# Optimization experiments

Hardware: AMD Instinct MI355X
Metric: run time of the kernel (lower is better)

The kernel has to match this reference:

```python
import jax, jax.numpy as jnp
import numpy as np
import math

B, T, C = 2, 2048, 1024
NH = 16
HD = C // NH

def setup_inputs() -> dict:
    key = jax.random.key(0)
    ks = jax.random.split(key, 3)
    scale = 0.02
    return {
        "x": jax.random.normal(ks[0], (B, T, C), dtype=jnp.float32),
        "Wqkv": jax.random.normal(ks[1], (C, 3 * C), dtype=jnp.float32) * scale,
        "bqkv": jnp.zeros((3 * C,), dtype=jnp.float32),
        "Wproj": jax.random.normal(ks[2], (C, C), dtype=jnp.float32) * scale,
        "bproj": jnp.zeros((C,), dtype=jnp.float32),
    }

def reference(x, Wqkv, bqkv, Wproj, bproj):
    b, t, c = x.shape
    qkv = x @ Wqkv + bqkv                      # (B,T,3C)
    qkv = qkv.reshape(b, t, 3, NH, HD)
    q = jnp.transpose(qkv[:, :, 0], (0, 2, 1, 3))  # (B,H,T,D)
    k = jnp.transpose(qkv[:, :, 1], (0, 2, 1, 3))
    v = jnp.transpose(qkv[:, :, 2], (0, 2, 1, 3))
    att = jnp.einsum('bhqd,bhkd->bhqk', q, k) / math.sqrt(HD)
    causal = jnp.tril(jnp.ones((t, t), dtype=bool))
    att = jnp.where(causal[None, None], att, jnp.float32(-jnp.inf))
    att = jax.nn.softmax(att, axis=-1)
    y = jnp.einsum('bhqk,bhkd->bhqd', att, v)  # (B,H,T,D)
    y = jnp.transpose(y, (0, 2, 1, 3)).reshape(b, t, c)
    return y @ Wproj + bproj
```

## Files before the change

kernel.cpp:

```cpp
#include <hip/hip_runtime.h>


typedef __attribute__((ext_vector_type(8))) short short8;
typedef __attribute__((ext_vector_type(4))) short short4v;
typedef __attribute__((ext_vector_type(4))) float f32x4;
typedef __attribute__((ext_vector_type(2))) unsigned int u32x2;

#define MFMA16(a, b, c) __builtin_amdgcn_mfma_f32_16x16x32_bf16((a), (b), (c), 0, 0, 0)
#define MFMA16K16(a, b, c) __builtin_amdgcn_mfma_f32_16x16x16bf16_1k((a), (b), (c), 0, 0, 0)

__device__ __forceinline__ unsigned short f2bf(float f) {
  unsigned u = __builtin_bit_cast(unsigned, f);
  u += 0x7fffu + ((u >> 16) & 1u);
  return (unsigned short)(u >> 16);
}

__device__ __forceinline__ unsigned short f2bf_fast(float f) {
  return (unsigned short)((__builtin_bit_cast(unsigned, f) + 0x8000u) >> 16);
}

#if __has_builtin(__builtin_amdgcn_cvt_pk_bf16_f32)
typedef __attribute__((ext_vector_type(2))) __bf16 bf16x2;
__device__ __forceinline__ short4v pack_bf16x4(float a, float b, float c, float d) {
  bf16x2 lo = __builtin_amdgcn_cvt_pk_bf16_f32(a, b);
  bf16x2 hi = __builtin_amdgcn_cvt_pk_bf16_f32(c, d);
  u32x2 t;
  t[0] = __builtin_bit_cast(unsigned, lo);
  t[1] = __builtin_bit_cast(unsigned, hi);
  return __builtin_bit_cast(short4v, t);
}
#else
__device__ __forceinline__ short4v pack_bf16x4(float a, float b, float c, float d) {
  short4v r;
  r[0] = (short)f2bf_fast(a); r[1] = (short)f2bf_fast(b);
  r[2] = (short)f2bf_fast(c); r[3] = (short)f2bf_fast(d);
  return r;
}
#endif

__device__ __forceinline__ short4v pack_rne4(float a, float b, float c, float d) {
  short4v r;
  r[0] = (short)f2bf(a); r[1] = (short)f2bf(b);
  r[2] = (short)f2bf(c); r[3] = (short)f2bf(d);
  return r;
}

__device__ __forceinline__ void gl2lds16(const void* g, void* l) {
  __builtin_amdgcn_global_load_lds(
      (__attribute__((address_space(1))) void*)g,
      (__attribute__((address_space(3))) void*)l,
      16, 0, 0);
}

__global__ __launch_bounds__(256)
void prep(const float* __restrict__ x, unsigned short* __restrict__ xb,
          const float* __restrict__ Wqkv, unsigned short* __restrict__ wqkvT,
          const float* __restrict__ Wproj, unsigned short* __restrict__ wprojT) {
  __shared__ float tile[64][65];
  const int bx = blockIdx.x, tid = threadIdx.x;
  if (bx < 4096) {
    const int i = (bx * 256 + tid) * 4;
    float4 f = *(const float4*)(x + i);
    unsigned long long r = (unsigned long long)f2bf(f.x)
        | ((unsigned long long)f2bf(f.y) << 16)
        | ((unsigned long long)f2bf(f.z) << 32)
        | ((unsigned long long)f2bf(f.w) << 48);
    *(unsigned long long*)(xb + i) = r;
    return;
  }
  const float* W;
  unsigned short* WT;
  int n0, k0, N;
  if (bx < 4864) {
    const int idx = bx - 4096;
    W = Wqkv; WT = wqkvT; N = 3072;
    n0 = (idx % 48) * 64; k0 = (idx / 48) * 64;
  } else {
    const int idx = bx - 4864;
    W = Wproj; WT = wprojT; N = 1024;
    n0 = (idx % 16) * 64; k0 = (idx / 16) * 64;
  }
  const int K = 1024;
  const int c = tid & 63, rbase = tid >> 6;
#pragma unroll
  for (int i = 0; i < 16; ++i) {
    int r = i * 4 + rbase;
    tile[r][c] = W[(size_t)(k0 + r) * N + n0 + c];
  }
  __syncthreads();
#pragma unroll
  for (int i = 0; i < 16; ++i) {
    int r = i * 4 + rbase;
    WT[(size_t)(n0 + r) * K + k0 + c] = f2bf(tile[c][r]);
  }
}

template <int MT>
__device__ __forceinline__ void gemm_core(
    const unsigned short* __restrict__ gA,
    const unsigned short* __restrict__ gB,
    unsigned short* As, unsigned short* Bs,
    int Kdim, int wave, int quad, int lr, int wm, int wn,
    f32x4 (&acc)[MT / 32][4]) {
  constexpr int IF = MT / 32;
  constexpr int RA = MT / 32;
  const size_t rstep = (size_t)32 * Kdim;
  for (int k0 = 0; k0 < Kdim; k0 += 64) {
#pragma unroll
    for (int rd = 0; rd < RA; ++rd)
      gl2lds16(gA + k0 + rd * rstep, As + rd * 2048 + wave * 512);
#pragma unroll
    for (int rd = 0; rd < 4; ++rd)
      gl2lds16(gB + k0 + rd * rstep, Bs + rd * 2048 + wave * 512);
    __syncthreads();
#pragma unroll
    for (int s = 0; s < 2; ++s) {
      const int sw = ((s * 4 + quad) ^ (lr & 7)) * 8;
      short8 a[IF], b[4];
#pragma unroll
      for (int i = 0; i < IF; ++i)
        a[i] = *(const short8*)(As + (wm * (MT / 2) + i * 16 + lr) * 64 + sw);
#pragma unroll
      for (int j = 0; j < 4; ++j)
        b[j] = *(const short8*)(Bs + (wn * 64 + j * 16 + lr) * 64 + sw);
#pragma unroll
      for (int i = 0; i < IF; ++i)
#pragma unroll
        for (int j = 0; j < 4; ++j)
          acc[i][j] = MFMA16(a[i], b[j], acc[i][j]);
    }
    __syncthreads();
  }
}

template <int EPI, int MT>
__global__ __launch_bounds__(256)
void gemm_bt(const unsigned short* __restrict__ A,
             const unsigned short* __restrict__ BT,
             const float* __restrict__ bias,
             float* __restrict__ outF,
             unsigned short* __restrict__ q_out,
             unsigned short* __restrict__ k_out,
             unsigned short* __restrict__ vT_out,
             int Ndim, int Kdim) {
  constexpr int IF = MT / 32;
  __shared__ __align__(16) unsigned short As[MT * 64];
  __shared__ __align__(16) unsigned short Bs[128 * 64];
  const int tid = threadIdx.x;
  const int wave = tid >> 6, lane = tid & 63;
  const int quad = lane >> 4, lr = lane & 15;
  const int wm = wave >> 1, wn = wave & 1;
  const int m0 = blockIdx.y * MT, n0 = blockIdx.x * 128;

  const int r_l = tid >> 3;
  const int cg = (tid & 7) ^ (r_l & 7);
  const unsigned short* gA = A + (size_t)(m0 + r_l) * Kdim + cg * 8;
  const unsigned short* gB = BT + (size_t)(n0 + r_l) * Kdim + cg * 8;

  f32x4 acc[IF][4] = {};
  gemm_core<MT>(gA, gB, As, Bs, Kdim, wave, quad, lr, wm, wn, acc);

  const int row_t = wm * (MT / 2) + quad * 4;
  const int col_t = wn * 64 + lr;
  if constexpr (EPI == 0) {
    const int sec = n0 >> 10;
    const float scl = (sec == 0) ? 0.18033688f : 1.0f;
#pragma unroll
    for (int j = 0; j < 4; ++j) {
      const int n = n0 + col_t + j * 16;
      const float bi = bias[n];
      const int nn = n & 1023, h = nn >> 6, d = nn & 63;
#pragma unroll
      for (int i = 0; i < IF; ++i) {
        const int m_base = m0 + row_t + i * 16;
        const int bb = m_base >> 11, t0 = m_base & 2047;
        const int bh = bb * 16 + h;
        if (sec == 2) {
          short4v pk = pack_rne4(acc[i][j][0] + bi, acc[i][j][1] + bi,
                                 acc[i][j][2] + bi, acc[i][j][3] + bi);
          *(short4v*)(vT_out + ((size_t)bh * 64 + d) * 2048 + t0) = pk;
        } else {
          unsigned short* dst = (sec == 0 ? q_out : k_out) + (size_t)bh * 131072 + t0 * 64 + d;
#pragma unroll
          for (int r = 0; r < 4; ++r)
            dst[r * 64] = f2bf((acc[i][j][r] + bi) * scl);
        }
      }
    }
  } else {
#pragma unroll
    for (int i = 0; i < IF; ++i)
#pragma unroll
      for (int r = 0; r < 4; ++r) {
        const int m = m0 + row_t + i * 16 + r;
#pragma unroll
        for (int j = 0; j < 4; ++j) {
          const int n = n0 + col_t + j * 16;
          outF[(size_t)m * Ndim + n] = acc[i][j][r] + bias[n];
        }
      }
  }
}

__global__ __launch_bounds__(256, 4)
void attn(const unsigned short* __restrict__ qbuf,
          const unsigned short* __restrict__ kbuf,
          const unsigned short* __restrict__ vT,
          unsigned short* __restrict__ yb,
          float* __restrict__ o_part,
          float* __restrict__ l_part) {
  __shared__ __align__(16) unsigned short Ks[2][4096];
  __shared__ __align__(16) unsigned short Vs[2][4096];
  const int tid = threadIdx.x, wave = tid >> 6, lane = tid & 63;
  const int quad = lane >> 4, lr = lane & 15;
  const int bh = blockIdx.x;
  const int jj = 47 - (int)blockIdx.y;
  int qt, kstart, kend, chunk;
  if (jj >= 32)      { qt = jj - 16; chunk = 1; kstart = (qt + 1) >> 1; kend = qt + 1; }
  else if (jj >= 16) { qt = jj;      chunk = 0; kstart = 0; kend = (qt + 1) >> 1; }
  else               { qt = jj;      chunk = -1; kstart = 0; kend = qt + 1; }
  const int qrow0 = qt * 64;

  const unsigned short* qp0 = qbuf + (size_t)bh * 131072;
  const unsigned short* kp0 = kbuf + (size_t)bh * 131072;
  const unsigned short* vp0 = vT   + (size_t)bh * 131072;

  short8 aq[2];
  {
    const unsigned short* qp =
        qp0 + (size_t)(qrow0 + wave * 16 + lr) * 64 + quad * 8;
    aq[0] = *(const short8*)qp;
    aq[1] = *(const short8*)(qp + 32);
  }

  short4v ones4;
#pragma unroll
  for (int i = 0; i < 4; ++i) ones4[i] = (short)0x3F80;

  const int sr = tid >> 3;
  const int scg = (tid & 7) ^ (sr & 7);
  int kbase[2];
#pragma unroll
  for (int h = 0; h < 2; ++h)
    kbase[h] = lr * 64 + (((quad + 4 * h) ^ (lr & 7)) << 3);
  int vbase[4];
#pragma unroll
  for (int kb = 0; kb < 4; ++kb)
    vbase[kb] = lr * 64 + (((2 * kb + (quad >> 1)) ^ (lr & 7)) << 3) + (quad & 1) * 4;

  f32x4 o[4] = {};
  f32x4 lacc = {};

  auto stage = [&](int buf, int kt) {
    const unsigned short* kg = kp0 + (size_t)(kt * 64 + sr) * 64 + scg * 8;
    const unsigned short* vg = vp0 + (size_t)sr * 2048 + kt * 64 + scg * 8;
    gl2lds16(kg,             &Ks[buf][wave * 512]);
    gl2lds16(kg + 32 * 64,   &Ks[buf][2048 + wave * 512]);
    gl2lds16(vg,             &Vs[buf][wave * 512]);
    gl2lds16(vg + 32 * 2048, &Vs[buf][2048 + wave * 512]);
  };

  stage(0, kstart);
  int cur = 0;
  for (int kt = kstart; kt < kend; ++kt) {
    __builtin_amdgcn_s_waitcnt(0x0F70);
    __builtin_amdgcn_s_barrier();
    if (kt + 1 < kend) stage(cur ^ 1, kt + 1);
    const unsigned short* Kb = Ks[cur];
    const unsigned short* Vb = Vs[cur];
    short8 bk[4][2];
#pragma unroll
    for (int jt = 0; jt < 4; ++jt) {
      bk[jt][0] = *(const short8*)(Kb + jt * 1024 + kbase[0]);
      bk[jt][1] = *(const short8*)(Kb + jt * 1024 + kbase[1]);
    }
    f32x4 s[4] = {};
    __builtin_amdgcn_s_setprio(1);
#pragma unroll
    for (int jt = 0; jt < 4; ++jt) {
      s[jt] = MFMA16(bk[jt][0], aq[0], s[jt]);
      s[jt] = MFMA16(bk[jt][1], aq[1], s[jt]);
    }
    __builtin_amdgcn_s_setprio(0);
    short4v pa[4];
    if (kt == qt) {
      const int qloc = wave * 16 + lr;
#pragma unroll
      for (int jt = 0; jt < 4; ++jt) {
        float p[4];
#pragma unroll
        for (int r = 0; r < 4; ++r) {
          p[r] = __builtin_amdgcn_exp2f(s[jt][r]);
          if (jt * 16 + quad * 4 + r > qloc) p[r] = 0.f;
        }
        pa[jt] = pack_bf16x4(p[0], p[1], p[2], p[3]);
      }
    } else {
#pragma unroll
      for (int jt = 0; jt < 4; ++jt) {
        float p[4];
#pragma unroll
        for (int r = 0; r < 4; ++r) p[r] = __builtin_amdgcn_exp2f(s[jt][r]);
        pa[jt] = pack_bf16x4(p[0], p[1], p[2], p[3]);
      }
    }
    __builtin_amdgcn_s_setprio(1);
#pragma unroll
    for (int kb = 0; kb < 4; ++kb)
      lacc = MFMA16K16(ones4, pa[kb], lacc);
#pragma unroll
    for (int kb = 0; kb < 4; ++kb)
#pragma unroll
      for (int jd = 0; jd < 4; ++jd) {
        const short4v bv = *(const short4v*)(Vb + jd * 1024 + vbase[kb]);
        o[jd] = MFMA16K16(pa[kb], bv, o[jd]);
      }
    __builtin_amdgcn_s_setprio(0);
    cur ^= 1;
  }

  if (chunk < 0) {
    const int b = bh >> 4, h = bh & 15;
    float inv[4];
#pragma unroll
    for (int r = 0; r < 4; ++r)
      inv[r] = __builtin_amdgcn_rcpf(__shfl(lacc[0], quad * 4 + r));
#pragma unroll
    for (int jd = 0; jd < 4; ++jd)
#pragma unroll
      for (int r = 0; r < 4; ++r) {
        const int t = qrow0 + wave * 16 + quad * 4 + r;
        yb[((size_t)b * 2048 + t) * 1024 + h * 64 + jd * 16 + lr] =
            f2bf(o[jd][r] * inv[r]);
      }
  } else {
    const int slot = (bh * 16 + (qt - 16)) * 2 + chunk;
    float* op = o_part + ((size_t)slot * 64 + wave * 16) * 64;
#pragma unroll
    for (int jd = 0; jd < 4; ++jd)
#pragma unroll
      for (int r = 0; r < 4; ++r)
        op[(quad * 4 + r) * 64 + jd * 16 + lr] = o[jd][r];
    if (lane < 16) l_part[slot * 64 + wave * 16 + lane] = lacc[0];
  }
}

__global__ __launch_bounds__(256)
void combine(const float* __restrict__ o_part, const float* __restrict__ l_part,
             unsigned short* __restrict__ yb) {
  const int bh = blockIdx.x, qtl = blockIdx.y;
  const int tid = threadIdx.x;
  const int row = tid >> 2, dd = (tid & 3) * 16;
  const int qt = 16 + qtl;
  const int slotA = (bh * 16 + qtl) * 2, slotB = slotA + 1;
  const float l = l_part[slotA * 64 + row] + l_part[slotB * 64 + row];
  const float inv = __builtin_amdgcn_rcpf(l);
  const float* oa = o_part + ((size_t)slotA * 64 + row) * 64 + dd;
  const float* ob = o_part + ((size_t)slotB * 64 + row) * 64 + dd;
  const int b = bh >> 4, h = bh & 15;
  unsigned short* yp = yb + ((size_t)b * 2048 + qt * 64 + row) * 1024 + h * 64 + dd;
#pragma unroll
  for (int j = 0; j < 16; j += 4) {
    const float4 a4 = *(const float4*)(oa + j);
    const float4 b4 = *(const float4*)(ob + j);
    short4v pk = pack_rne4((a4.x + b4.x) * inv, (a4.y + b4.y) * inv,
                           (a4.z + b4.z) * inv, (a4.w + b4.w) * inv);
    *(short4v*)(yp + j) = pk;
  }
}

extern "C" void kernel_launch(void* const* d_in, const int* in_sizes, int n_in,
                              void* d_out, int out_size, void* d_ws, size_t ws_size,
                              hipStream_t stream) {
  const float* x     = (const float*)d_in[0];
  const float* Wqkv  = (const float*)d_in[1];
  const float* bqkv  = (const float*)d_in[2];
  const float* Wproj = (const float*)d_in[3];
  const float* bproj = (const float*)d_in[4];
  float* out = (float*)d_out;

  char* ws = (char*)d_ws;
  unsigned short* xb     = (unsigned short*)(ws);
  unsigned short* wqkvT  = (unsigned short*)(ws + 8388608);
  unsigned short* wprojT = (unsigned short*)(ws + 14680064);
  unsigned short* qbuf   = (unsigned short*)(ws + 16777216);
  unsigned short* kbuf   = (unsigned short*)(ws + 25165824);
  unsigned short* vTbuf  = (unsigned short*)(ws + 33554432);
  unsigned short* ybuf   = (unsigned short*)(ws + 41943040);
  float* o_part          = (float*)(ws + 50331648);
  float* l_part          = (float*)(ws + 67108864);

  prep<<<5120, 256, 0, stream>>>(x, xb, Wqkv, wqkvT, Wproj, wprojT);
  gemm_bt<0, 128><<<dim3(24, 32), 256, 0, stream>>>(xb, wqkvT, bqkv, nullptr,
                                                    qbuf, kbuf, vTbuf, 3072, 1024);
  attn<<<dim3(32, 48), 256, 0, stream>>>(qbuf, kbuf, vTbuf, ybuf, o_part, l_part);
  combine<<<dim3(32, 16), 256, 0, stream>>>(o_part, l_part, ybuf);
  gemm_bt<1, 64><<<dim3(8, 64), 256, 0, stream>>>(ybuf, wprojT, bproj, out,
                                                  nullptr, nullptr, nullptr, 1024, 1024);
}
```

Baseline: 176.9 us.

## Process 128 query rows per attention block and rebalance causal split-K chunks

Each attention block now handles two 64-row query groups that share every K/V tile staged in LDS, halving K/V traffic per query row. Work is split into 1 to 4 key-range chunks according to query-tile depth so blocks carry roughly equal causal work. Combine is generalized to sum a variable number of partials. In exchange the kernel needs more registers, even as the launch bounds now ask for 5 waves of occupancy, which may cause spills. It also adds a larger partial buffer and more combine traffic.

```diff
diff --git a/kernel.cpp b/kernel.cpp
--- a/kernel.cpp
+++ b/kernel.cpp
@@ -202,7 +202,7 @@
   }
 }
 
-__global__ __launch_bounds__(256, 4)
+__global__ __launch_bounds__(256, 5)
 void attn(const unsigned short* __restrict__ qbuf,
           const unsigned short* __restrict__ kbuf,
           const unsigned short* __restrict__ vT,
@@ -214,23 +214,28 @@
   const int tid = threadIdx.x, wave = tid >> 6, lane = tid & 63;
   const int quad = lane >> 4, lr = lane & 15;
   const int bh = blockIdx.x;
-  const int jj = 47 - (int)blockIdx.y;
-  int qt, kstart, kend, chunk;
-  if (jj >= 32)      { qt = jj - 16; chunk = 1; kstart = (qt + 1) >> 1; kend = qt + 1; }
-  else if (jj >= 16) { qt = jj;      chunk = 0; kstart = 0; kend = (qt + 1) >> 1; }
-  else               { qt = jj;      chunk = -1; kstart = 0; kend = qt + 1; }
-  const int qrow0 = qt * 64;
+  const int by = blockIdx.y;
+  int qt, ci, nch;
+  if (by < 16)      { qt = 12 + (by & 3); ci = by >> 2; nch = 4; }
+  else if (by < 28) { int u = by - 16; qt = 8 + (u & 3); ci = u >> 2; nch = 3; }
+  else if (by < 36) { int u = by - 28; qt = 4 + (u & 3); ci = u >> 2; nch = 2; }
+  else              { qt = by - 36; ci = 0; nch = 1; }
+  const int nt = 2 * qt + 2;
+  const int kstart = (ci * nt) / nch;
+  const int kend = ((ci + 1) * nt) / nch;
+  const int qrow0 = qt * 128;
 
   const unsigned short* qp0 = qbuf + (size_t)bh * 131072;
   const unsigned short* kp0 = kbuf + (size_t)bh * 131072;
   const unsigned short* vp0 = vT   + (size_t)bh * 131072;
 
-  short8 aq[2];
-  {
+  short8 aq[2][2];
+#pragma unroll
+  for (int g = 0; g < 2; ++g) {
     const unsigned short* qp =
-        qp0 + (size_t)(qrow0 + wave * 16 + lr) * 64 + quad * 8;
-    aq[0] = *(const short8*)qp;
-    aq[1] = *(const short8*)(qp + 32);
+        qp0 + (size_t)(qrow0 + g * 64 + wave * 16 + lr) * 64 + quad * 8;
+    aq[g][0] = *(const short8*)qp;
+    aq[g][1] = *(const short8*)(qp + 32);
   }
 
   short4v ones4;
@@ -248,8 +253,8 @@
   for (int kb = 0; kb < 4; ++kb)
     vbase[kb] = lr * 64 + (((2 * kb + (quad >> 1)) ^ (lr & 7)) << 3) + (quad & 1) * 4;
 
-  f32x4 o[4] = {};
-  f32x4 lacc = {};
+  f32x4 o[2][4] = {};
+  f32x4 lacc[2] = {};
 
   auto stage = [&](int buf, int kt) {
     const unsigned short* kg = kp0 + (size_t)(kt * 64 + sr) * 64 + scg * 8;
@@ -260,6 +265,7 @@
     gl2lds16(vg + 32 * 2048, &Vs[buf][2048 + wave * 512]);
   };
 
+  const int d0 = 2 * qt;
   stage(0, kstart);
   int cur = 0;
   for (int kt = kstart; kt < kend; ++kt) {
@@ -274,97 +280,127 @@
       bk[jt][0] = *(const short8*)(Kb + jt * 1024 + kbase[0]);
       bk[jt][1] = *(const short8*)(Kb + jt * 1024 + kbase[1]);
     }
-    f32x4 s[4] = {};
+    short4v pa[2][4];
+#pragma unroll
+    for (int g = 0; g < 2; ++g) {
+      const int dg = 2 * qt + g;
+      if (kt > dg) {
+#pragma unroll
+        for (int jt = 0; jt < 4; ++jt) pa[g][jt] = (short4v)0;
+      } else {
+        f32x4 s[4] = {};
+        __builtin_amdgcn_s_setprio(1);
+#pragma unroll
+        for (int jt = 0; jt < 4; ++jt) {
+          s[jt] = MFMA16(bk[jt][0], aq[g][0], s[jt]);
+          s[jt] = MFMA16(bk[jt][1], aq[g][1], s[jt]);
+        }
+        __builtin_amdgcn_s_setprio(0);
+        if (kt == dg) {
+          const int qloc = wave * 16 + lr;
+#pragma unroll
+          for (int jt = 0; jt < 4; ++jt) {
+            float p[4];
+#pragma unroll
+            for (int r = 0; r < 4; ++r) {
+              p[r] = __builtin_amdgcn_exp2f(s[jt][r]);
+              if (jt * 16 + quad * 4 + r > qloc) p[r] = 0.f;
+            }
+            pa[g][jt] = pack_bf16x4(p[0], p[1], p[2], p[3]);
+          }
+        } else {
+#pragma unroll
+          for (int jt = 0; jt < 4; ++jt) {
+            float p[4];
+#pragma unroll
+            for (int r = 0; r < 4; ++r) p[r] = __builtin_amdgcn_exp2f(s[jt][r]);
+            pa[g][jt] = pack_bf16x4(p[0], p[1], p[2], p[3]);
+          }
+        }
+        __builtin_amdgcn_s_setprio(1);
+#pragma unroll
+        for (int kb = 0; kb < 4; ++kb)
+          lacc[g] = MFMA16K16(ones4, pa[g][kb], lacc[g]);
+        __builtin_amdgcn_s_setprio(0);
+      }
+    }
     __builtin_amdgcn_s_setprio(1);
-#pragma unroll
-    for (int jt = 0; jt < 4; ++jt) {
-      s[jt] = MFMA16(bk[jt][0], aq[0], s[jt]);
-      s[jt] = MFMA16(bk[jt][1], aq[1], s[jt]);
-    }
-    __builtin_amdgcn_s_setprio(0);
-    short4v pa[4];
-    if (kt == qt) {
-      const int qloc = wave * 16 + lr;
-#pragma unroll
-      for (int jt = 0; jt < 4; ++jt) {
-        float p[4];
-#pragma unroll
-        for (int r = 0; r < 4; ++r) {
-          p[r] = __builtin_amdgcn_exp2f(s[jt][r]);
-          if (jt * 16 + quad * 4 + r > qloc) p[r] = 0.f;
-        }
-        pa[jt] = pack_bf16x4(p[0], p[1], p[2], p[3]);
-      }
+    if (kt <= d0) {
+#pragma unroll
+      for (int kb = 0; kb < 4; ++kb)
+#pragma unroll
+        for (int jd = 0; jd < 4; ++jd) {
+          const short4v bv = *(const short4v*)(Vb + jd * 1024 + vbase[kb]);
+          o[0][jd] = MFMA16K16(pa[0][kb], bv, o[0][jd]);
+          o[1][jd] = MFMA16K16(pa[1][kb], bv, o[1][jd]);
+        }
     } else {
 #pragma unroll
-      for (int jt = 0; jt < 4; ++jt) {
-        float p[4];
-#pragma unroll
-        for (int r = 0; r < 4; ++r) p[r] = __builtin_amdgcn_exp2f(s[jt][r]);
-        pa[jt] = pack_bf16x4(p[0], p[1], p[2], p[3]);
-      }
-    }
-    __builtin_amdgcn_s_setprio(1);
-#pragma unroll
-    for (int kb = 0; kb < 4; ++kb)
-      lacc = MFMA16K16(ones4, pa[kb], lacc);
-#pragma unroll
-    for (int kb = 0; kb < 4; ++kb)
-#pragma unroll
-      for (int jd = 0; jd < 4; ++jd) {
-        const short4v bv = *(const short4v*)(Vb + jd * 1024 + vbase[kb]);
-        o[jd] = MFMA16K16(pa[kb], bv, o[jd]);
-      }
+      for (int kb = 0; kb < 4; ++kb)
+#pragma unroll
+        for (int jd = 0; jd < 4; ++jd) {
+          const short4v bv = *(const short4v*)(Vb + jd * 1024 + vbase[kb]);
+          o[1][jd] = MFMA16K16(pa[1][kb], bv, o[1][jd]);
+        }
+    }
     __builtin_amdgcn_s_setprio(0);
     cur ^= 1;
   }
 
-  if (chunk < 0) {
+  if (nch == 1) {
     const int b = bh >> 4, h = bh & 15;
-    float inv[4];
-#pragma unroll
-    for (int r = 0; r < 4; ++r)
-      inv[r] = __builtin_amdgcn_rcpf(__shfl(lacc[0], quad * 4 + r));
-#pragma unroll
-    for (int jd = 0; jd < 4; ++jd)
-#pragma unroll
-      for (int r = 0; r < 4; ++r) {
-        const int t = qrow0 + wave * 16 + quad * 4 + r;
-        yb[((size_t)b * 2048 + t) * 1024 + h * 64 + jd * 16 + lr] =
-            f2bf(o[jd][r] * inv[r]);
-      }
+#pragma unroll
+    for (int g = 0; g < 2; ++g) {
+      float inv[4];
+#pragma unroll
+      for (int r = 0; r < 4; ++r)
+        inv[r] = __builtin_amdgcn_rcpf(__shfl(lacc[g][0], quad * 4 + r));
+#pragma unroll
+      for (int jd = 0; jd < 4; ++jd)
+#pragma unroll
+        for (int r = 0; r < 4; ++r) {
+          const int t = qrow0 + g * 64 + wave * 16 + quad * 4 + r;
+          yb[((size_t)b * 2048 + t) * 1024 + h * 64 + jd * 16 + lr] =
+              f2bf(o[g][jd][r] * inv[r]);
+        }
+    }
   } else {
-    const int slot = (bh * 16 + (qt - 16)) * 2 + chunk;
-    float* op = o_part + ((size_t)slot * 64 + wave * 16) * 64;
-#pragma unroll
-    for (int jd = 0; jd < 4; ++jd)
-#pragma unroll
-      for (int r = 0; r < 4; ++r)
-        op[(quad * 4 + r) * 64 + jd * 16 + lr] = o[jd][r];
-    if (lane < 16) l_part[slot * 64 + wave * 16 + lane] = lacc[0];
+    const int slot = (bh * 16 + qt) * 4 + ci;
+    float* op = o_part + (size_t)slot * 8192;
+#pragma unroll
+    for (int g = 0; g < 2; ++g) {
+#pragma unroll
+      for (int jd = 0; jd < 4; ++jd)
+#pragma unroll
+        for (int r = 0; r < 4; ++r)
+          op[(g * 64 + wave * 16 + quad * 4 + r) * 64 + jd * 16 + lr] = o[g][jd][r];
+      if (lane < 16)
+        l_part[slot * 128 + g * 64 + wave * 16 + lane] = lacc[g][0];
+    }
   }
 }
 
 __global__ __launch_bounds__(256)
 void combine(const float* __restrict__ o_part, const float* __restrict__ l_part,
              unsigned short* __restrict__ yb) {
-  const int bh = blockIdx.x, qtl = blockIdx.y;
+  const int bh = blockIdx.x, qt = 4 + (int)blockIdx.y;
+  const int nch = (qt >= 12) ? 4 : (qt >= 8 ? 3 : 2);
   const int tid = threadIdx.x;
-  const int row = tid >> 2, dd = (tid & 3) * 16;
-  const int qt = 16 + qtl;
-  const int slotA = (bh * 16 + qtl) * 2, slotB = slotA + 1;
-  const float l = l_part[slotA * 64 + row] + l_part[slotB * 64 + row];
+  const int row = tid >> 1, dd = (tid & 1) * 32;
+  const int slot0 = (bh * 16 + qt) * 4;
+  float l = 0.f;
+  for (int ci = 0; ci < nch; ++ci) l += l_part[(slot0 + ci) * 128 + row];
   const float inv = __builtin_amdgcn_rcpf(l);
-  const float* oa = o_part + ((size_t)slotA * 64 + row) * 64 + dd;
-  const float* ob = o_part + ((size_t)slotB * 64 + row) * 64 + dd;
   const int b = bh >> 4, h = bh & 15;
-  unsigned short* yp = yb + ((size_t)b * 2048 + qt * 64 + row) * 1024 + h * 64 + dd;
-#pragma unroll
-  for (int j = 0; j < 16; j += 4) {
-    const float4 a4 = *(const float4*)(oa + j);
-    const float4 b4 = *(const float4*)(ob + j);
-    short4v pk = pack_rne4((a4.x + b4.x) * inv, (a4.y + b4.y) * inv,
-                           (a4.z + b4.z) * inv, (a4.w + b4.w) * inv);
+  unsigned short* yp = yb + ((size_t)b * 2048 + qt * 128 + row) * 1024 + h * 64 + dd;
+#pragma unroll
+  for (int j = 0; j < 32; j += 4) {
+    float sx = 0.f, sy = 0.f, sz = 0.f, sw = 0.f;
+    for (int ci = 0; ci < nch; ++ci) {
+      const float4 a4 = *(const float4*)(o_part + ((size_t)(slot0 + ci) * 128 + row) * 64 + dd + j);
+      sx += a4.x; sy += a4.y; sz += a4.z; sw += a4.w;
+    }
+    short4v pk = pack_rne4(sx * inv, sy * inv, sz * inv, sw * inv);
     *(short4v*)(yp + j) = pk;
   }
 }
@@ -388,13 +424,13 @@
   unsigned short* vTbuf  = (unsigned short*)(ws + 33554432);
   unsigned short* ybuf   = (unsigned short*)(ws + 41943040);
   float* o_part          = (float*)(ws + 50331648);
-  float* l_part          = (float*)(ws + 67108864);
+  float* l_part          = (float*)(ws + 117440512);
 
   prep<<<5120, 256, 0, stream>>>(x, xb, Wqkv, wqkvT, Wproj, wprojT);
   gemm_bt<0, 128><<<dim3(24, 32), 256, 0, stream>>>(xb, wqkvT, bqkv, nullptr,
                                                     qbuf, kbuf, vTbuf, 3072, 1024);
-  attn<<<dim3(32, 48), 256, 0, stream>>>(qbuf, kbuf, vTbuf, ybuf, o_part, l_part);
-  combine<<<dim3(32, 16), 256, 0, stream>>>(o_part, l_part, ybuf);
+  attn<<<dim3(32, 40), 256, 0, stream>>>(qbuf, kbuf, vTbuf, ybuf, o_part, l_part);
+  combine<<<dim3(32, 12), 256, 0, stream>>>(o_part, l_part, ybuf);
   gemm_bt<1, 64><<<dim3(8, 64), 256, 0, stream>>>(ybuf, wprojT, bproj, out,
                                                   nullptr, nullptr, nullptr, 1024, 1024);
 }
```

New measurement: 265.7 us. 1.5x slower.

## Split causal attention KV range into up to four chunks for load balance

Applied to the files above, without the earlier changes.

Replaces the two-way KV split for the upper half of the query tiles with a graded split: query tiles 8-15 get two chunks, 16-23 three, and 24-31 four, while tiles 0-7 stay whole. This makes per-block work more uniform and raises the attn grid from 48 to 80 blocks per head. The combine kernel now sums a variable number of partials over tiles 8-31. The cost is more partial-output traffic to global memory, a larger workspace region, and a heavier combine pass.

```diff
diff --git a/kernel.cpp b/kernel.cpp
--- a/kernel.cpp
+++ b/kernel.cpp
@@ -214,11 +214,15 @@
   const int tid = threadIdx.x, wave = tid >> 6, lane = tid & 63;
   const int quad = lane >> 4, lr = lane & 15;
   const int bh = blockIdx.x;
-  const int jj = 47 - (int)blockIdx.y;
-  int qt, kstart, kend, chunk;
-  if (jj >= 32)      { qt = jj - 16; chunk = 1; kstart = (qt + 1) >> 1; kend = qt + 1; }
-  else if (jj >= 16) { qt = jj;      chunk = 0; kstart = 0; kend = (qt + 1) >> 1; }
-  else               { qt = jj;      chunk = -1; kstart = 0; kend = qt + 1; }
+  const int d = (int)blockIdx.y;
+  int qt, ci, nch;
+  if (d < 32)      { qt = 24 + (d & 7); ci = d >> 3; nch = 4; }
+  else if (d < 56) { int u = d - 32; qt = 16 + (u & 7); ci = u >> 3; nch = 3; }
+  else if (d < 72) { int u = d - 56; qt = 8 + (u & 7); ci = u >> 3; nch = 2; }
+  else             { qt = d - 72; ci = 0; nch = 1; }
+  const int nt = qt + 1;
+  const int kstart = (ci * nt) / nch;
+  const int kend = ((ci + 1) * nt) / nch;
   const int qrow0 = qt * 64;
 
   const unsigned short* qp0 = qbuf + (size_t)bh * 131072;
@@ -319,7 +323,7 @@
     cur ^= 1;
   }
 
-  if (chunk < 0) {
+  if (nch == 1) {
     const int b = bh >> 4, h = bh & 15;
     float inv[4];
 #pragma unroll
@@ -334,7 +338,7 @@
             f2bf(o[jd][r] * inv[r]);
       }
   } else {
-    const int slot = (bh * 16 + (qt - 16)) * 2 + chunk;
+    const int slot = (bh * 32 + qt) * 4 + ci;
     float* op = o_part + ((size_t)slot * 64 + wave * 16) * 64;
 #pragma unroll
     for (int jd = 0; jd < 4; ++jd)
@@ -348,23 +352,24 @@
 __global__ __launch_bounds__(256)
 void combine(const float* __restrict__ o_part, const float* __restrict__ l_part,
              unsigned short* __restrict__ yb) {
-  const int bh = blockIdx.x, qtl = blockIdx.y;
+  const int bh = blockIdx.x, qt = 8 + (int)blockIdx.y;
+  const int nch = (qt >> 3) + 1;
   const int tid = threadIdx.x;
   const int row = tid >> 2, dd = (tid & 3) * 16;
-  const int qt = 16 + qtl;
-  const int slotA = (bh * 16 + qtl) * 2, slotB = slotA + 1;
-  const float l = l_part[slotA * 64 + row] + l_part[slotB * 64 + row];
+  const int slot0 = (bh * 32 + qt) * 4;
+  float l = 0.f;
+  for (int ci = 0; ci < nch; ++ci) l += l_part[(slot0 + ci) * 64 + row];
   const float inv = __builtin_amdgcn_rcpf(l);
-  const float* oa = o_part + ((size_t)slotA * 64 + row) * 64 + dd;
-  const float* ob = o_part + ((size_t)slotB * 64 + row) * 64 + dd;
   const int b = bh >> 4, h = bh & 15;
   unsigned short* yp = yb + ((size_t)b * 2048 + qt * 64 + row) * 1024 + h * 64 + dd;
 #pragma unroll
   for (int j = 0; j < 16; j += 4) {
-    const float4 a4 = *(const float4*)(oa + j);
-    const float4 b4 = *(const float4*)(ob + j);
-    short4v pk = pack_rne4((a4.x + b4.x) * inv, (a4.y + b4.y) * inv,
-                           (a4.z + b4.z) * inv, (a4.w + b4.w) * inv);
+    float sx = 0.f, sy = 0.f, sz = 0.f, sw = 0.f;
+    for (int ci = 0; ci < nch; ++ci) {
+      const float4 a4 = *(const float4*)(o_part + ((size_t)(slot0 + ci) * 64 + row) * 64 + dd + j);
+      sx += a4.x; sy += a4.y; sz += a4.z; sw += a4.w;
+    }
+    short4v pk = pack_rne4(sx * inv, sy * inv, sz * inv, sw * inv);
     *(short4v*)(yp + j) = pk;
   }
 }
@@ -388,13 +393,13 @@
   unsigned short* vTbuf  = (unsigned short*)(ws + 33554432);
   unsigned short* ybuf   = (unsigned short*)(ws + 41943040);
   float* o_part          = (float*)(ws + 50331648);
-  float* l_part          = (float*)(ws + 67108864);
+  float* l_part          = (float*)(ws + 117440512);
 
   prep<<<5120, 256, 0, stream>>>(x, xb, Wqkv, wqkvT, Wproj, wprojT);
   gemm_bt<0, 128><<<dim3(24, 32), 256, 0, stream>>>(xb, wqkvT, bqkv, nullptr,
                                                     qbuf, kbuf, vTbuf, 3072, 1024);
-  attn<<<dim3(32, 48), 256, 0, stream>>>(qbuf, kbuf, vTbuf, ybuf, o_part, l_part);
-  combine<<<dim3(32, 16), 256, 0, stream>>>(o_part, l_part, ybuf);
+  attn<<<dim3(32, 80), 256, 0, stream>>>(qbuf, kbuf, vTbuf, ybuf, o_part, l_part);
+  combine<<<dim3(32, 24), 256, 0, stream>>>(o_part, l_part, ybuf);
   gemm_bt<1, 64><<<dim3(8, 64), 256, 0, stream>>>(ybuf, wprojT, bproj, out,
                                                   nullptr, nullptr, nullptr, 1024, 1024);
 }
```

Result: slower. 190.7 us (+7.8%).
